# Kernel tuning notes

Measured on AMD Instinct MI355X. Metric: run time of the kernel, lower is better.

## Reference

```python
import jax, jax.numpy as jnp
import numpy as np

T = 5          # Newton-Schulz iterations
EPS = 1e-05


def reference(X):
    # X: (B, C, L); training-mode IterNorm whitening with num_groups=1
    B, C, L = X.shape
    x = jnp.transpose(X, (1, 0, 2)).reshape(C, -1)        # (d, m)
    d, m = x.shape
    mean = jnp.mean(x, axis=-1, keepdims=True)
    xc = x - mean                                         # (d, m)
    I = jnp.eye(d, dtype=X.dtype)
    Sigma = I * EPS + (xc @ xc.T) * (1.0 / m)             # (d, d)
    rTr = 1.0 / jnp.trace(Sigma)                          # scalar
    Sigma_N = Sigma * rTr
    P = I
    for _ in range(T):
        P = 1.5 * P - 0.5 * (P @ P @ P) @ Sigma_N
    wm = P * jnp.sqrt(rTr)                                # whitening matrix
    xn = wm @ xc                                          # (d, m)
    Xn = jnp.transpose(xn.reshape(C, B, L), (1, 0, 2))
    return Xn


def setup_inputs() -> dict:
    key = jax.random.key(0)
    X = jax.random.normal(key, (32, 64, 8192), dtype=jnp.float32)
    return {"X": X}
```

## Files before the change

kernel.cpp:

```cpp
#include <hip/hip_runtime.h>
#include <math.h>

#define L_DIM   8192
#define NCH     64
#define M_TOT_F 262144.0f
#define EPS_F   1e-5f
#define GBLK    512
#define GTPB    8
#define ABLK    512
#define ATPB    8

typedef float f32x4 __attribute__((ext_vector_type(4)));
typedef short bf16x8 __attribute__((ext_vector_type(8)));

union U8 { unsigned u[4]; bf16x8 v; };

__device__ __forceinline__ void cvt2(float f0, float f1, unsigned& h, unsigned& l) {
    unsigned u0 = __float_as_uint(f0), u1 = __float_as_uint(f1);
    h = (u0 >> 16) | (u1 & 0xFFFF0000u);
    float r0 = f0 - __uint_as_float(u0 & 0xFFFF0000u);
    float r1 = f1 - __uint_as_float(u1 & 0xFFFF0000u);
    l = (__float_as_uint(r0) >> 16) | (__float_as_uint(r1) & 0xFFFF0000u);
}

__device__ __forceinline__ void split16(float v, unsigned short& h, unsigned short& l) {
    unsigned u = __float_as_uint(v);
    h = (unsigned short)(u >> 16);
    float r = v - __uint_as_float(u & 0xFFFF0000u);
    l = (unsigned short)(__float_as_uint(r) >> 16);
}

__device__ __forceinline__ float b2f(unsigned short h) {
    return __uint_as_float(((unsigned)h) << 16);
}

__device__ __forceinline__ f32x4 mfma16(bf16x8 a, bf16x8 b, f32x4 c) {
    return __builtin_amdgcn_mfma_f32_16x16x32_bf16(a, b, c, 0, 0, 0);
}

__device__ __forceinline__ f32x4 fzero() {
    f32x4 z; z[0] = 0.f; z[1] = 0.f; z[2] = 0.f; z[3] = 0.f; return z;
}

__global__ __launch_bounds__(256) void gram_kernel(const float* __restrict__ X,
                                                   float* __restrict__ ws) {
    __shared__ __align__(16) unsigned short hfrag[2][4096];
    __shared__ __align__(16) unsigned short lfrag[2][4096];
    const int tid  = threadIdx.x;
    const int w    = tid >> 6;
    const int lane = tid & 63;
    const int m    = lane & 15;
    const int q    = lane >> 4;
    const int row  = 16 * w + m;

    f32x4 acc1[4], acc2[4];
#pragma unroll
    for (int nb = 0; nb < 4; ++nb) { acc1[nb] = fzero(); acc2[nb] = fzero(); }
    float sacc = 0.f;

    const int tile0 = blockIdx.x * GTPB;
    float4 v[4];
    {
        int t0 = tile0;
        const float* src = X + ((size_t)((t0 >> 7) * NCH + row)) * L_DIM + ((t0 & 127) << 6) + 8 * q;
        v[0] = *(const float4*)(src);
        v[1] = *(const float4*)(src + 4);
        v[2] = *(const float4*)(src + 32);
        v[3] = *(const float4*)(src + 36);
    }

    for (int t = 0; t < GTPB; ++t) {
        const int p = t & 1;
#pragma unroll
        for (int i = 0; i < 4; ++i) sacc += v[i].x + v[i].y + v[i].z + v[i].w;

        bf16x8 Ah[2], Al[2];
#pragma unroll
        for (int k = 0; k < 2; ++k) {
            U8 H, L;
            cvt2(v[2 * k].x,     v[2 * k].y,     H.u[0], L.u[0]);
            cvt2(v[2 * k].z,     v[2 * k].w,     H.u[1], L.u[1]);
            cvt2(v[2 * k + 1].x, v[2 * k + 1].y, H.u[2], L.u[2]);
            cvt2(v[2 * k + 1].z, v[2 * k + 1].w, H.u[3], L.u[3]);
            Ah[k] = H.v; Al[k] = L.v;
            int chunk = ((w * 2 + k) * 4 + q) * 16 + m;
            *(bf16x8*)&hfrag[p][chunk * 8] = H.v;
            *(bf16x8*)&lfrag[p][chunk * 8] = L.v;
        }

        if (t + 1 < GTPB) {
            int tn = tile0 + t + 1;
            const float* src = X + ((size_t)((tn >> 7) * NCH + row)) * L_DIM + ((tn & 127) << 6) + 8 * q;
            v[0] = *(const float4*)(src);
            v[1] = *(const float4*)(src + 4);
            v[2] = *(const float4*)(src + 32);
            v[3] = *(const float4*)(src + 36);
        }
        __syncthreads();

#pragma unroll
        for (int k = 0; k < 2; ++k)
#pragma unroll
            for (int nb = 0; nb < 4; ++nb) {
                int chunk = ((nb * 2 + k) * 4 + q) * 16 + m;
                bf16x8 bh = *(const bf16x8*)&hfrag[p][chunk * 8];
                bf16x8 bl = *(const bf16x8*)&lfrag[p][chunk * 8];
                acc1[nb] = mfma16(Ah[k], bh, acc1[nb]);
                acc2[nb] = mfma16(Ah[k], bl, acc2[nb]);
            }
    }

#pragma unroll
    for (int nb = 0; nb < 4; ++nb)
#pragma unroll
        for (int r = 0; r < 4; ++r) {
            int grow = 16 * w + 4 * q + r;
            int gcol = 16 * nb + m;
            atomicAdd(&ws[grow * 64 + gcol],        acc1[nb][r]);
            atomicAdd(&ws[4096 + grow * 64 + gcol], acc2[nb][r]);
        }
    sacc += __shfl_xor(sacc, 16);
    sacc += __shfl_xor(sacc, 32);
    if (q == 0) atomicAdd(&ws[8192 + row], sacc);
}

#define OFF_A      0
#define OFF_T1H    0
#define OFF_T1L    9216
#define OFF_T2H    18432
#define OFF_PH     32768
#define OFF_PL     41984
#define OFF_SH     51200
#define OFF_SL     60416
#define OFF_T2L    69632
#define OFF_MU     78848
#define OFF_SCAL   79104
#define SM_BYTES   79120

__device__ __forceinline__ void mm_core(f32x4* acc,
                                        const unsigned short* Xh, const unsigned short* Xl,
                                        const unsigned short* Yh, const unsigned short* Yl,
                                        int w, int m, int q) {
#pragma unroll
    for (int k0 = 0; k0 < 64; k0 += 32) {
        bf16x8 xh = *(const bf16x8*)&Xh[(16 * w + m) * 72 + k0 + 8 * q];
        bf16x8 xl = *(const bf16x8*)&Xl[(16 * w + m) * 72 + k0 + 8 * q];
#pragma unroll
        for (int nb = 0; nb < 4; ++nb) {
            bf16x8 yh = *(const bf16x8*)&Yh[(16 * nb + m) * 72 + k0 + 8 * q];
            bf16x8 yl = *(const bf16x8*)&Yl[(16 * nb + m) * 72 + k0 + 8 * q];
            acc[nb] = mfma16(xh, yh, acc[nb]);
            acc[nb] = mfma16(xh, yl, acc[nb]);
            acc[nb] = mfma16(xl, yh, acc[nb]);
        }
    }
}

__device__ __forceinline__ void mm_pl(unsigned short* Dh, unsigned short* Dl,
                                      const unsigned short* Xh, const unsigned short* Xl,
                                      const unsigned short* Yh, const unsigned short* Yl,
                                      int w, int m, int q) {
    f32x4 acc[4];
#pragma unroll
    for (int nb = 0; nb < 4; ++nb) acc[nb] = fzero();
    mm_core(acc, Xh, Xl, Yh, Yl, w, m, q);
#pragma unroll
    for (int nb = 0; nb < 4; ++nb)
#pragma unroll
        for (int r = 0; r < 4; ++r) {
            int row = 16 * w + 4 * q + r, col = 16 * nb + m;
            unsigned short h, l;
            split16(acc[nb][r], h, l);
            Dh[row * 72 + col] = h;
            Dl[row * 72 + col] = l;
        }
}

__global__ __launch_bounds__(256, 2) void nsapply_kernel(const float* __restrict__ X,
                                                         float* __restrict__ Y,
                                                         const float* __restrict__ ws) {
    __shared__ __align__(16) unsigned char smem[SM_BYTES];
    const int tid  = threadIdx.x;
    const int bid  = blockIdx.x;
    const int w    = tid >> 6;
    const int lane = tid & 63;
    const int m    = lane & 15;
    const int q    = lane >> 4;
    const int cp   = tid & 31;
    const int lg   = tid >> 5;

    unsigned short* hfrag = (unsigned short*)(smem + OFF_A);
    unsigned short* lfrag = (unsigned short*)(smem + OFF_A + 16384);
    unsigned short* Ph  = (unsigned short*)(smem + OFF_PH);
    unsigned short* Pl  = (unsigned short*)(smem + OFF_PL);
    unsigned short* Sh  = (unsigned short*)(smem + OFF_SH);
    unsigned short* Sl  = (unsigned short*)(smem + OFF_SL);
    unsigned short* T1h = (unsigned short*)(smem + OFF_T1H);
    unsigned short* T1l = (unsigned short*)(smem + OFF_T1L);
    unsigned short* T2h = (unsigned short*)(smem + OFF_T2H);
    unsigned short* T2l = (unsigned short*)(smem + OFF_T2L);
    float* mu   = (float*)(smem + OFF_MU);
    float* scal = (float*)(smem + OFF_SCAL);
    unsigned short* wmh = (unsigned short*)(smem + OFF_SH);
    unsigned short* wml = (unsigned short*)(smem + OFF_SL);
    float* bias = (float*)(smem + OFF_SH + 8192);
    const float inv_m = 1.0f / M_TOT_F;

    float4 va[2], vb[2];
    {
        int tile = bid * ATPB;
        const float* xb = X + (size_t)(tile >> 7) * (NCH * L_DIM) + ((tile & 127) << 6)
                          + (size_t)(2 * cp) * L_DIM + 4 * lg;
#pragma unroll
        for (int ss = 0; ss < 2; ++ss) {
            va[ss] = *(const float4*)(xb + 32 * ss);
            vb[ss] = *(const float4*)(xb + 32 * ss + L_DIM);
        }
    }

    if (tid < 64) mu[tid] = ws[8192 + tid] * inv_m;
    __syncthreads();

    if (tid < 64) {
        int e = tid * 65;
        float g  = (ws[e] + 2.0f * ws[4096 + e]) * inv_m;
        float sd = g - mu[tid] * mu[tid] + EPS_F;
#pragma unroll
        for (int off = 32; off >= 1; off >>= 1) sd += __shfl_xor(sd, off);
        if (tid == 0) { scal[0] = 1.0f / sd; scal[1] = sqrtf(1.0f / sd); }
    }
    __syncthreads();
    const float rTr = scal[0];

    for (int e = tid; e < 4096; e += 256) {
        int i = e >> 6, j = e & 63;
        float g   = (ws[e] + ws[4096 + e] + ws[4096 + (j << 6) + i]) * inv_m;
        float sig = g - mu[i] * mu[j] + ((i == j) ? EPS_F : 0.f);
        float sn  = sig * rTr;
        unsigned short h, l;
        split16(sn, h, l);
        Sh[i * 72 + j] = h; Sl[i * 72 + j] = l;
        float pv = ((i == j) ? 1.5f : 0.f) - 0.5f * sn;
        split16(pv, h, l);
        Ph[i * 72 + j] = h; Pl[i * 72 + j] = l;
    }
    __syncthreads();

    for (int it = 0; it < 4; ++it) {
        mm_pl(T1h, T1l, Ph, Pl, Ph, Pl, w, m, q);
        __syncthreads();
        mm_pl(T2h, T2l, T1h, T1l, Ph, Pl, w, m, q);
        __syncthreads();
        f32x4 acc[4];
#pragma unroll
        for (int nb = 0; nb < 4; ++nb) acc[nb] = fzero();
        mm_core(acc, T2h, T2l, Sh, Sl, w, m, q);
#pragma unroll
        for (int nb = 0; nb < 4; ++nb)
#pragma unroll
            for (int r = 0; r < 4; ++r) {
                int row = 16 * w + 4 * q + r, col = 16 * nb + m;
                int pidx = row * 72 + col;
                float pold = b2f(Ph[pidx]) + b2f(Pl[pidx]);
                float pv = 1.5f * pold - 0.5f * acc[nb][r];
                unsigned short h, l;
                split16(pv, h, l);
                Ph[pidx] = h; Pl[pidx] = l;
            }
        __syncthreads();
    }

    const float s = scal[1];
    if (tid < 64) {
        float a = 0.f;
#pragma unroll 8
        for (int k = 0; k < 64; ++k)
            a += (b2f(Ph[tid * 72 + k]) + b2f(Pl[tid * 72 + k])) * mu[k];
        bias[tid] = -a * s;
    }
    for (int e = tid; e < 4096; e += 256) {
        int i = e >> 6, j = e & 63;
        float v = (b2f(Ph[i * 72 + j]) + b2f(Pl[i * 72 + j])) * s;
        unsigned short h, l;
        split16(v, h, l);
        wmh[e] = h;
        wml[e] = l;
    }
    __syncthreads();

    bf16x8 Ah[2], Al[2];
#pragma unroll
    for (int kk = 0; kk < 2; ++kk) {
        Ah[kk] = *(const bf16x8*)&wmh[(16 * w + m) * 64 + 32 * kk + 8 * q];
        Al[kk] = *(const bf16x8*)&wml[(16 * w + m) * 64 + 32 * kk + 8 * q];
    }
    const float4 bias4 = *(const float4*)&bias[16 * w + 4 * q];

    for (int t = 0; t < ATPB; ++t) {
        int tile = bid * ATPB + t;
        int bidx = tile >> 7;
        int l0   = (tile & 127) << 6;
        const int p = t & 1;
        unsigned* hw2 = (unsigned*)(hfrag + p * 4096);
        unsigned* lw2 = (unsigned*)(lfrag + p * 4096);

#pragma unroll
        for (int ss = 0; ss < 2; ++ss) {
            float fa[4], fb[4];
            *(float4*)fa = va[ss];
            *(float4*)fb = vb[ss];
#pragma unroll
            for (int i = 0; i < 4; ++i) {
                int l = 4 * lg + 32 * ss + i;
                unsigned h, lo2;
                cvt2(fa[i], fb[i], h, lo2);
                int widx = l * 32 + (((cp >> 2) ^ (l & 7)) << 2) + (cp & 3);
                hw2[widx] = h;
                lw2[widx] = lo2;
            }
        }

        if (t + 1 < ATPB) {
            int tn = tile + 1;
            const float* xb = X + (size_t)(tn >> 7) * (NCH * L_DIM) + ((tn & 127) << 6)
                              + (size_t)(2 * cp) * L_DIM + 4 * lg;
#pragma unroll
            for (int ss = 0; ss < 2; ++ss) {
                va[ss] = *(const float4*)(xb + 32 * ss);
                vb[ss] = *(const float4*)(xb + 32 * ss + L_DIM);
            }
        }
        __syncthreads();

        f32x4 acc[4];
#pragma unroll
        for (int nb = 0; nb < 4; ++nb) {
            acc[nb][0] = bias4.x; acc[nb][1] = bias4.y;
            acc[nb][2] = bias4.z; acc[nb][3] = bias4.w;
        }
#pragma unroll
        for (int kk = 0; kk < 2; ++kk)
#pragma unroll
            for (int nb = 0; nb < 4; ++nb) {
                int l = 16 * nb + m;
                int saddr = l * 64 + ((((4 * kk + q) ^ (l & 7))) << 3);
                bf16x8 bh = *(const bf16x8*)&hfrag[p * 4096 + saddr];
                bf16x8 bl = *(const bf16x8*)&lfrag[p * 4096 + saddr];
                acc[nb] = mfma16(Ah[kk], bh, acc[nb]);
                acc[nb] = mfma16(Ah[kk], bl, acc[nb]);
                acc[nb] = mfma16(Al[kk], bh, acc[nb]);
            }

#pragma unroll
        for (int nb = 0; nb < 4; ++nb)
#pragma unroll
            for (int rr = 0; rr < 4; ++rr)
                Y[((size_t)bidx * NCH + 16 * w + 4 * q + rr) * L_DIM + l0 + 16 * nb + m] = acc[nb][rr];
    }
}

extern "C" void kernel_launch(void* const* d_in, const int* in_sizes, int n_in,
                              void* d_out, int out_size, void* d_ws, size_t ws_size,
                              hipStream_t stream) {
    const float* X = (const float*)d_in[0];
    float* Y  = (float*)d_out;
    float* ws = (float*)d_ws;

    hipMemsetAsync(ws, 0, 8256 * sizeof(float), stream);
    hipLaunchKernelGGL(gram_kernel,    dim3(GBLK), dim3(256), 0, stream, X, ws);
    hipLaunchKernelGGL(nsapply_kernel, dim3(ABLK), dim3(256), 0, stream, X, Y, ws);
}
```

Baseline: 163.8 us.

## Fuse gram and Newton-Schulz apply kernels into one persistent kernel with grid barriers

Merges the memset, the gram kernel and the apply kernel into a single launch of 512 blocks. A hierarchical software grid barrier orders zeroing, atomic accumulation and the read of the reduced statistics. The first X tile for the apply phase is prefetched before the second barrier, and the gram matrices are staged once into shared memory instead of being read from global memory repeatedly. This removes launch gaps and the memset, but relies on all 512 blocks being co-resident (two per CU) and adds barrier spin costs.

```diff
diff --git a/kernel.cpp b/kernel.cpp
--- a/kernel.cpp
+++ b/kernel.cpp
@@ -5,15 +5,58 @@
 #define NCH     64
 #define M_TOT_F 262144.0f
 #define EPS_F   1e-5f
-#define GBLK    512
+#define NBLK    512
+#define TPB     256
 #define GTPB    8
-#define ABLK    512
 #define ATPB    8
 
 typedef float f32x4 __attribute__((ext_vector_type(4)));
 typedef short bf16x8 __attribute__((ext_vector_type(8)));
 
 union U8 { unsigned u[4]; bf16x8 v; };
+
+#define OFF_A      0
+#define OFF_T1H    0
+#define OFF_T1L    9216
+#define OFF_T2H    18432
+#define OFF_G1     0
+#define OFF_G2P    16384
+#define OFF_PH     33024
+#define OFF_PL     42240
+#define OFF_SH     51456
+#define OFF_SL     60672
+#define OFF_T2L    69888
+#define OFF_MU     79104
+#define OFF_SCAL   79360
+#define SM_BYTES   79376
+
+__device__ unsigned swb_cnt[8 * 32];
+__device__ unsigned swb_root;
+__device__ unsigned swb_gen;
+
+__device__ __forceinline__ void grid_barrier(int bid) {
+    __syncthreads();
+    if (threadIdx.x == 0) {
+        __threadfence();
+        unsigned mygen = __hip_atomic_load(&swb_gen, __ATOMIC_ACQUIRE, __HIP_MEMORY_SCOPE_AGENT);
+        int g = bid & 7;
+        unsigned o = __hip_atomic_fetch_add(&swb_cnt[g * 32], 1u, __ATOMIC_ACQ_REL, __HIP_MEMORY_SCOPE_AGENT);
+        if (o == (NBLK / 8 - 1)) {
+            unsigned r = __hip_atomic_fetch_add(&swb_root, 1u, __ATOMIC_ACQ_REL, __HIP_MEMORY_SCOPE_AGENT);
+            if (r == 7) {
+#pragma unroll
+                for (int i = 0; i < 8; ++i)
+                    __hip_atomic_store(&swb_cnt[i * 32], 0u, __ATOMIC_RELAXED, __HIP_MEMORY_SCOPE_AGENT);
+                __hip_atomic_store(&swb_root, 0u, __ATOMIC_RELAXED, __HIP_MEMORY_SCOPE_AGENT);
+                __hip_atomic_fetch_add(&swb_gen, 1u, __ATOMIC_RELEASE, __HIP_MEMORY_SCOPE_AGENT);
+            }
+        }
+        while (__hip_atomic_load(&swb_gen, __ATOMIC_ACQUIRE, __HIP_MEMORY_SCOPE_AGENT) == mygen)
+            __builtin_amdgcn_s_sleep(2);
+        __threadfence();
+    }
+    __syncthreads();
+}
 
 __device__ __forceinline__ void cvt2(float f0, float f1, unsigned& h, unsigned& l) {
     unsigned u0 = __float_as_uint(f0), u1 = __float_as_uint(f1);
@@ -34,6 +77,10 @@
     return __uint_as_float(((unsigned)h) << 16);
 }
 
+__device__ __forceinline__ float aload(const float* p) {
+    return __hip_atomic_load(p, __ATOMIC_RELAXED, __HIP_MEMORY_SCOPE_AGENT);
+}
+
 __device__ __forceinline__ f32x4 mfma16(bf16x8 a, bf16x8 b, f32x4 c) {
     return __builtin_amdgcn_mfma_f32_16x16x32_bf16(a, b, c, 0, 0, 0);
 }
@@ -41,101 +88,6 @@
 __device__ __forceinline__ f32x4 fzero() {
     f32x4 z; z[0] = 0.f; z[1] = 0.f; z[2] = 0.f; z[3] = 0.f; return z;
 }
-
-__global__ __launch_bounds__(256) void gram_kernel(const float* __restrict__ X,
-                                                   float* __restrict__ ws) {
-    __shared__ __align__(16) unsigned short hfrag[2][4096];
-    __shared__ __align__(16) unsigned short lfrag[2][4096];
-    const int tid  = threadIdx.x;
-    const int w    = tid >> 6;
-    const int lane = tid & 63;
-    const int m    = lane & 15;
-    const int q    = lane >> 4;
-    const int row  = 16 * w + m;
-
-    f32x4 acc1[4], acc2[4];
-#pragma unroll
-    for (int nb = 0; nb < 4; ++nb) { acc1[nb] = fzero(); acc2[nb] = fzero(); }
-    float sacc = 0.f;
-
-    const int tile0 = blockIdx.x * GTPB;
-    float4 v[4];
-    {
-        int t0 = tile0;
-        const float* src = X + ((size_t)((t0 >> 7) * NCH + row)) * L_DIM + ((t0 & 127) << 6) + 8 * q;
-        v[0] = *(const float4*)(src);
-        v[1] = *(const float4*)(src + 4);
-        v[2] = *(const float4*)(src + 32);
-        v[3] = *(const float4*)(src + 36);
-    }
-
-    for (int t = 0; t < GTPB; ++t) {
-        const int p = t & 1;
-#pragma unroll
-        for (int i = 0; i < 4; ++i) sacc += v[i].x + v[i].y + v[i].z + v[i].w;
-
-        bf16x8 Ah[2], Al[2];
-#pragma unroll
-        for (int k = 0; k < 2; ++k) {
-            U8 H, L;
-            cvt2(v[2 * k].x,     v[2 * k].y,     H.u[0], L.u[0]);
-            cvt2(v[2 * k].z,     v[2 * k].w,     H.u[1], L.u[1]);
-            cvt2(v[2 * k + 1].x, v[2 * k + 1].y, H.u[2], L.u[2]);
-            cvt2(v[2 * k + 1].z, v[2 * k + 1].w, H.u[3], L.u[3]);
-            Ah[k] = H.v; Al[k] = L.v;
-            int chunk = ((w * 2 + k) * 4 + q) * 16 + m;
-            *(bf16x8*)&hfrag[p][chunk * 8] = H.v;
-            *(bf16x8*)&lfrag[p][chunk * 8] = L.v;
-        }
-
-        if (t + 1 < GTPB) {
-            int tn = tile0 + t + 1;
-            const float* src = X + ((size_t)((tn >> 7) * NCH + row)) * L_DIM + ((tn & 127) << 6) + 8 * q;
-            v[0] = *(const float4*)(src);
-            v[1] = *(const float4*)(src + 4);
-            v[2] = *(const float4*)(src + 32);
-            v[3] = *(const float4*)(src + 36);
-        }
-        __syncthreads();
-
-#pragma unroll
-        for (int k = 0; k < 2; ++k)
-#pragma unroll
-            for (int nb = 0; nb < 4; ++nb) {
-                int chunk = ((nb * 2 + k) * 4 + q) * 16 + m;
-                bf16x8 bh = *(const bf16x8*)&hfrag[p][chunk * 8];
-                bf16x8 bl = *(const bf16x8*)&lfrag[p][chunk * 8];
-                acc1[nb] = mfma16(Ah[k], bh, acc1[nb]);
-                acc2[nb] = mfma16(Ah[k], bl, acc2[nb]);
-            }
-    }
-
-#pragma unroll
-    for (int nb = 0; nb < 4; ++nb)
-#pragma unroll
-        for (int r = 0; r < 4; ++r) {
-            int grow = 16 * w + 4 * q + r;
-            int gcol = 16 * nb + m;
-            atomicAdd(&ws[grow * 64 + gcol],        acc1[nb][r]);
-            atomicAdd(&ws[4096 + grow * 64 + gcol], acc2[nb][r]);
-        }
-    sacc += __shfl_xor(sacc, 16);
-    sacc += __shfl_xor(sacc, 32);
-    if (q == 0) atomicAdd(&ws[8192 + row], sacc);
-}
-
-#define OFF_A      0
-#define OFF_T1H    0
-#define OFF_T1L    9216
-#define OFF_T2H    18432
-#define OFF_PH     32768
-#define OFF_PL     41984
-#define OFF_SH     51200
-#define OFF_SL     60416
-#define OFF_T2L    69632
-#define OFF_MU     78848
-#define OFF_SCAL   79104
-#define SM_BYTES   79120
 
 __device__ __forceinline__ void mm_core(f32x4* acc,
                                         const unsigned short* Xh, const unsigned short* Xl,
@@ -176,12 +128,13 @@
         }
 }
 
-__global__ __launch_bounds__(256, 2) void nsapply_kernel(const float* __restrict__ X,
-                                                         float* __restrict__ Y,
-                                                         const float* __restrict__ ws) {
+__global__ __launch_bounds__(TPB, 2) void mega_kernel(const float* __restrict__ X,
+                                                      float* __restrict__ Y,
+                                                      float* __restrict__ ws) {
     __shared__ __align__(16) unsigned char smem[SM_BYTES];
+
+    const int bid  = blockIdx.x;
     const int tid  = threadIdx.x;
-    const int bid  = blockIdx.x;
     const int w    = tid >> 6;
     const int lane = tid & 63;
     const int m    = lane & 15;
@@ -191,6 +144,104 @@
 
     unsigned short* hfrag = (unsigned short*)(smem + OFF_A);
     unsigned short* lfrag = (unsigned short*)(smem + OFF_A + 16384);
+
+    if (tid < 17) {
+        int g = bid * 17 + tid;
+        if (g < 8256)
+            __hip_atomic_store(&ws[g], 0.0f, __ATOMIC_RELAXED, __HIP_MEMORY_SCOPE_AGENT);
+    }
+
+    f32x4 acc1[4], acc2[4];
+#pragma unroll
+    for (int nb = 0; nb < 4; ++nb) { acc1[nb] = fzero(); acc2[nb] = fzero(); }
+    float sacc = 0.f;
+    {
+        const int row = 16 * w + m;
+        const int tile0 = bid * GTPB;
+        float4 v[4];
+        {
+            int t0 = tile0;
+            const float* src = X + ((size_t)((t0 >> 7) * NCH + row)) * L_DIM + ((t0 & 127) << 6) + 8 * q;
+            v[0] = *(const float4*)(src);
+            v[1] = *(const float4*)(src + 4);
+            v[2] = *(const float4*)(src + 32);
+            v[3] = *(const float4*)(src + 36);
+        }
+
+        for (int t = 0; t < GTPB; ++t) {
+            const int p = t & 1;
+#pragma unroll
+            for (int i = 0; i < 4; ++i) sacc += v[i].x + v[i].y + v[i].z + v[i].w;
+
+            bf16x8 Ah[2], Al[2];
+#pragma unroll
+            for (int k = 0; k < 2; ++k) {
+                U8 H, L;
+                cvt2(v[2 * k].x,     v[2 * k].y,     H.u[0], L.u[0]);
+                cvt2(v[2 * k].z,     v[2 * k].w,     H.u[1], L.u[1]);
+                cvt2(v[2 * k + 1].x, v[2 * k + 1].y, H.u[2], L.u[2]);
+                cvt2(v[2 * k + 1].z, v[2 * k + 1].w, H.u[3], L.u[3]);
+                Ah[k] = H.v; Al[k] = L.v;
+                int chunk = ((w * 2 + k) * 4 + q) * 16 + m;
+                *(bf16x8*)&hfrag[p * 4096 + chunk * 8] = H.v;
+                *(bf16x8*)&lfrag[p * 4096 + chunk * 8] = L.v;
+            }
+
+            if (t + 1 < GTPB) {
+                int tn = tile0 + t + 1;
+                const float* src = X + ((size_t)((tn >> 7) * NCH + row)) * L_DIM + ((tn & 127) << 6) + 8 * q;
+                v[0] = *(const float4*)(src);
+                v[1] = *(const float4*)(src + 4);
+                v[2] = *(const float4*)(src + 32);
+                v[3] = *(const float4*)(src + 36);
+            }
+            __syncthreads();
+
+#pragma unroll
+            for (int k = 0; k < 2; ++k)
+#pragma unroll
+                for (int nb = 0; nb < 4; ++nb) {
+                    int chunk = ((nb * 2 + k) * 4 + q) * 16 + m;
+                    bf16x8 bh = *(const bf16x8*)&hfrag[p * 4096 + chunk * 8];
+                    bf16x8 bl = *(const bf16x8*)&lfrag[p * 4096 + chunk * 8];
+                    acc1[nb] = mfma16(Ah[k], bh, acc1[nb]);
+                    acc2[nb] = mfma16(Ah[k], bl, acc2[nb]);
+                }
+        }
+    }
+
+    grid_barrier(bid);
+
+    {
+        const int row = 16 * w + m;
+#pragma unroll
+        for (int nb = 0; nb < 4; ++nb)
+#pragma unroll
+            for (int r = 0; r < 4; ++r) {
+                int grow = 16 * w + 4 * q + r;
+                int gcol = 16 * nb + m;
+                atomicAdd(&ws[grow * 64 + gcol],        acc1[nb][r]);
+                atomicAdd(&ws[4096 + grow * 64 + gcol], acc2[nb][r]);
+            }
+        sacc += __shfl_xor(sacc, 16);
+        sacc += __shfl_xor(sacc, 32);
+        if (q == 0) atomicAdd(&ws[8192 + row], sacc);
+    }
+
+    float4 va[2], vb[2];
+    {
+        int tile = bid * ATPB;
+        const float* xb = X + (size_t)(tile >> 7) * (NCH * L_DIM) + ((tile & 127) << 6)
+                          + (size_t)(2 * cp) * L_DIM + 4 * lg;
+#pragma unroll
+        for (int ss = 0; ss < 2; ++ss) {
+            va[ss] = *(const float4*)(xb + 32 * ss);
+            vb[ss] = *(const float4*)(xb + 32 * ss + L_DIM);
+        }
+    }
+
+    grid_barrier(bid);
+
     unsigned short* Ph  = (unsigned short*)(smem + OFF_PH);
     unsigned short* Pl  = (unsigned short*)(smem + OFF_PL);
     unsigned short* Sh  = (unsigned short*)(smem + OFF_SH);
@@ -204,26 +255,20 @@
     unsigned short* wmh = (unsigned short*)(smem + OFF_SH);
     unsigned short* wml = (unsigned short*)(smem + OFF_SL);
     float* bias = (float*)(smem + OFF_SH + 8192);
+    float* G1f  = (float*)(smem + OFF_G1);
+    float* G2p  = (float*)(smem + OFF_G2P);
     const float inv_m = 1.0f / M_TOT_F;
 
-    float4 va[2], vb[2];
-    {
-        int tile = bid * ATPB;
-        const float* xb = X + (size_t)(tile >> 7) * (NCH * L_DIM) + ((tile & 127) << 6)
-                          + (size_t)(2 * cp) * L_DIM + 4 * lg;
-#pragma unroll
-        for (int ss = 0; ss < 2; ++ss) {
-            va[ss] = *(const float4*)(xb + 32 * ss);
-            vb[ss] = *(const float4*)(xb + 32 * ss + L_DIM);
-        }
-    }
-
-    if (tid < 64) mu[tid] = ws[8192 + tid] * inv_m;
+    for (int e = tid; e < 4096; e += 256) {
+        int i = e >> 6, j = e & 63;
+        G1f[e]          = aload(&ws[e]);
+        G2p[i * 65 + j] = aload(&ws[4096 + e]);
+    }
+    if (tid < 64) mu[tid] = aload(&ws[8192 + tid]) * inv_m;
     __syncthreads();
 
     if (tid < 64) {
-        int e = tid * 65;
-        float g  = (ws[e] + 2.0f * ws[4096 + e]) * inv_m;
+        float g  = (G1f[tid * 65] + 2.0f * G2p[tid * 66]) * inv_m;
         float sd = g - mu[tid] * mu[tid] + EPS_F;
 #pragma unroll
         for (int off = 32; off >= 1; off >>= 1) sd += __shfl_xor(sd, off);
@@ -234,7 +279,7 @@
 
     for (int e = tid; e < 4096; e += 256) {
         int i = e >> 6, j = e & 63;
-        float g   = (ws[e] + ws[4096 + e] + ws[4096 + (j << 6) + i]) * inv_m;
+        float g   = (G1f[e] + G2p[i * 65 + j] + G2p[j * 65 + i]) * inv_m;
         float sig = g - mu[i] * mu[j] + ((i == j) ? EPS_F : 0.f);
         float sn  = sig * rTr;
         unsigned short h, l;
@@ -288,11 +333,11 @@
     }
     __syncthreads();
 
-    bf16x8 Ah[2], Al[2];
+    bf16x8 Ah2[2], Al2[2];
 #pragma unroll
     for (int kk = 0; kk < 2; ++kk) {
-        Ah[kk] = *(const bf16x8*)&wmh[(16 * w + m) * 64 + 32 * kk + 8 * q];
-        Al[kk] = *(const bf16x8*)&wml[(16 * w + m) * 64 + 32 * kk + 8 * q];
+        Ah2[kk] = *(const bf16x8*)&wmh[(16 * w + m) * 64 + 32 * kk + 8 * q];
+        Al2[kk] = *(const bf16x8*)&wml[(16 * w + m) * 64 + 32 * kk + 8 * q];
     }
     const float4 bias4 = *(const float4*)&bias[16 * w + 4 * q];
 
@@ -346,9 +391,9 @@
                 int saddr = l * 64 + ((((4 * kk + q) ^ (l & 7))) << 3);
                 bf16x8 bh = *(const bf16x8*)&hfrag[p * 4096 + saddr];
                 bf16x8 bl = *(const bf16x8*)&lfrag[p * 4096 + saddr];
-                acc[nb] = mfma16(Ah[kk], bh, acc[nb]);
-                acc[nb] = mfma16(Ah[kk], bl, acc[nb]);
-                acc[nb] = mfma16(Al[kk], bh, acc[nb]);
+                acc[nb] = mfma16(Ah2[kk], bh, acc[nb]);
+                acc[nb] = mfma16(Ah2[kk], bl, acc[nb]);
+                acc[nb] = mfma16(Al2[kk], bh, acc[nb]);
             }
 
 #pragma unroll
@@ -365,8 +410,5 @@
     const float* X = (const float*)d_in[0];
     float* Y  = (float*)d_out;
     float* ws = (float*)d_ws;
-
-    hipMemsetAsync(ws, 0, 8256 * sizeof(float), stream);
-    hipLaunchKernelGGL(gram_kernel,    dim3(GBLK), dim3(256), 0, stream, X, ws);
-    hipLaunchKernelGGL(nsapply_kernel, dim3(ABLK), dim3(256), 0, stream, X, Y, ws);
-}
+    hipLaunchKernelGGL(mega_kernel, dim3(NBLK), dim3(TPB), 0, stream, X, Y, ws);
+}
```

Result: slower. 268.5 us (+64.0%).
